# Optimization experiments

Measured on AMD Instinct MI355X. Metric: run time of the kernel, lower is better.

The kernel has to match this reference:

```python
import jax, jax.numpy as jnp
import numpy as np

B, S, V, E, H, C = 64, 512, 30000, 300, 256, 32


def setup_inputs() -> dict:
    key = jax.random.key(0)
    ks = jax.random.split(key, 12)
    g = 0.02
    return dict(
        tokens=jax.random.randint(ks[0], (B, S), 1, V),
        lengths=jax.random.randint(ks[1], (B,), S // 2, S + 1),
        targets=jax.random.randint(ks[2], (B, S), 0, C),
        emb=jax.random.normal(ks[3], (V, E), jnp.float32) * g,
        Wf=jax.random.normal(ks[4], (E, 4 * H), jnp.float32) * g,
        Uf=jax.random.normal(ks[5], (H, 4 * H), jnp.float32) * g,
        bf=jnp.zeros((4 * H,), jnp.float32),
        Wb=jax.random.normal(ks[6], (E, 4 * H), jnp.float32) * g,
        Ub=jax.random.normal(ks[7], (H, 4 * H), jnp.float32) * g,
        bb=jnp.zeros((4 * H,), jnp.float32),
        Wd=jax.random.normal(ks[8], (2 * H, C), jnp.float32) * g,
        bd=jnp.zeros((C,), jnp.float32),
        trans=jax.random.uniform(ks[9], (C, C), jnp.float32),
    )


def _lstm(x, W, U, b):
    # x: [B,S,E] -> hidden sequence [B,S,H]; Keras gate order i,f,g(cand),o
    xproj = jnp.einsum('bse,eh->bsh', x, W) + b  # precompute input projection

    def step(carry, xp):  # xp: [B,4H]
        h, c = carry
        z = xp + h @ U
        i, f, g, o = jnp.split(z, 4, axis=-1)
        c = jax.nn.sigmoid(f) * c + jax.nn.sigmoid(i) * jnp.tanh(g)
        h = jax.nn.sigmoid(o) * jnp.tanh(c)
        return (h, c), h

    h0 = jnp.zeros((x.shape[0], U.shape[0]), x.dtype)
    _, hs = jax.lax.scan(step, (h0, h0), jnp.swapaxes(xproj, 0, 1))
    return jnp.swapaxes(hs, 0, 1)


def _crf_log_likelihood(logits, targets, lengths, trans):
    # tfa.text.crf_log_likelihood: sequence score minus log partition (forward algorithm)
    mask = jnp.arange(S)[None, :] < lengths[:, None]  # [B,S]
    maskf = mask.astype(logits.dtype)
    unary = jnp.take_along_axis(logits, targets[..., None], axis=2)[..., 0]  # [B,S]
    unary = jnp.sum(unary * maskf, axis=1)
    binary = trans[targets[:, :-1], targets[:, 1:]] * maskf[:, 1:]  # valid where t+1 < length
    binary = jnp.sum(binary, axis=1)

    alpha0 = logits[:, 0]  # [B,C] (lengths >= 1)

    def step(alpha, inp):
        logit_t, m_t = inp  # [B,C], [B]
        new = jax.nn.logsumexp(alpha[:, :, None] + trans[None], axis=1) + logit_t
        return jnp.where(m_t[:, None], new, alpha), None

    alpha, _ = jax.lax.scan(
        step, alpha0,
        (jnp.swapaxes(logits[:, 1:], 0, 1), jnp.swapaxes(mask[:, 1:], 0, 1)))
    log_norm = jax.nn.logsumexp(alpha, axis=-1)
    return unary + binary - log_norm


def reference(tokens, lengths, targets, emb, Wf, Uf, bf, Wb, Ub, bb, Wd, bd, trans):
    x = emb[tokens]                         # [B,S,E]; dropout is identity at inference
    hf = _lstm(x, Wf, Uf, bf)               # forward direction
    hb = _lstm(x[:, ::-1], Wb, Ub, bb)[:, ::-1]  # backward direction
    h = jnp.concatenate([hf, hb], axis=-1)  # [B,S,2H]
    logits = h @ Wd + bd                    # [B,S,C]
    ll = _crf_log_likelihood(logits, targets, lengths, trans)
    return logits, ll, trans
```

## Files before the change

### kernel.cpp

```cpp
#include <hip/hip_runtime.h>

#define Bdim 64
#define Sdim 512
#define Vdim 30000
#define Edim 300
#define Hdim 256
#define Cdim 32
#define G4   1024
#define NROW 32768
#define KQ   32
#define USTAGE 9
#define RKQ    12
#define EPAIR  (Edim / 2)
#define KCH    5

typedef _Float16 half2v __attribute__((ext_vector_type(2)));
typedef _Float16 f16x8  __attribute__((ext_vector_type(8)));
typedef float    f32x4  __attribute__((ext_vector_type(4)));
typedef unsigned int u32x4 __attribute__((ext_vector_type(4)));

__device__ __forceinline__ unsigned short f2h_bits(float f) {
    union { _Float16 h; unsigned short u; } v; v.h = (_Float16)f; return v.u;
}
__device__ __forceinline__ float h2f(unsigned short u) {
    union { _Float16 h; unsigned short u; } v; v.u = u; return (float)v.h;
}
__device__ __forceinline__ unsigned int pack2h(float lo, float hi) {
    return (unsigned int)f2h_bits(lo) | ((unsigned int)f2h_bits(hi) << 16);
}
__device__ __forceinline__ float sigf(float x) { return 1.0f / (1.0f + __expf(-x)); }
__device__ __forceinline__ float tanhfast(float x) { return 2.0f / (1.0f + __expf(-2.0f * x)) - 1.0f; }

__device__ __forceinline__ float dot2(unsigned int u, unsigned int h, float acc) {
#if __has_builtin(__builtin_amdgcn_fdot2)
    union { unsigned int i; half2v h; } a, b; a.i = u; b.i = h;
    return __builtin_amdgcn_fdot2(a.h, b.h, acc, false);
#else
    acc = fmaf(h2f((unsigned short)(u & 0xffffu)), h2f((unsigned short)(h & 0xffffu)), acc);
    return fmaf(h2f((unsigned short)(u >> 16)), h2f((unsigned short)(h >> 16)), acc);
#endif
}
__device__ __forceinline__ void dot8(float& a0, float& a1, u32x4 uv, u32x4 hv) {
    a0 = dot2(uv.x, hv.x, a0);
    a1 = dot2(uv.y, hv.y, a1);
    a0 = dot2(uv.z, hv.z, a0);
    a1 = dot2(uv.w, hv.w, a1);
}

__global__ __launch_bounds__(256) void k_pack_u8(
    const float* __restrict__ Uf, const float* __restrict__ Ub,
    unsigned short* __restrict__ upk8)
{
    int idx = blockIdx.x * 256 + threadIdx.x;
    if (idx >= 2 * KQ * 1024) return;
    int dir = idx >> 15;
    int rem = idx & 32767;
    int kq  = rem >> 10;
    int n   = rem & 1023;
    const float* U = dir ? Ub : Uf;
    unsigned int w[4];
    #pragma unroll
    for (int p = 0; p < 4; ++p)
        w[p] = pack2h(U[(8 * kq + 2 * p) * G4 + n], U[(8 * kq + 2 * p + 1) * G4 + n]);
    uint4 o = make_uint4(w[0], w[1], w[2], w[3]);
    *(uint4*)&upk8[(size_t)idx * 8] = o;
}

__global__ __launch_bounds__(256) void k_pack_emb(
    const float* __restrict__ emb, unsigned int* __restrict__ embp)
{
    int p = blockIdx.x * 256 + threadIdx.x;
    if (p >= Vdim * EPAIR) return;
    float2 v = *(const float2*)&emb[(size_t)2 * p];
    embp[p] = pack2h(v.x, v.y);
}

__global__ __launch_bounds__(256) void k_pack_w(
    const float* __restrict__ Wf, const float* __restrict__ Wb,
    unsigned int* __restrict__ Wp)
{
    int idx = blockIdx.x * 256 + threadIdx.x;
    if (idx >= 2 * EPAIR * 1024) return;
    int dir = idx / (EPAIR * 1024);
    int rem = idx - dir * (EPAIR * 1024);
    int kp  = rem >> 10;
    int n   = rem & 1023;
    const float* W = dir ? Wb : Wf;
    Wp[idx] = pack2h(W[(2 * kp) * G4 + n], W[(2 * kp + 1) * G4 + n]);
}

__global__ __launch_bounds__(256) void k_pack_wd(
    const float* __restrict__ Wd, unsigned int* __restrict__ WdP)
{
    int i = blockIdx.x * 256 + threadIdx.x;
    if (i >= 256 * 32) return;
    int kp = i >> 5, c = i & 31;
    WdP[i] = pack2h(Wd[(2 * kp) * 32 + c], Wd[(2 * kp + 1) * 32 + c]);
}

__global__ __launch_bounds__(256, 4) void k_xproj(
    const int* __restrict__ tokens, const unsigned int* __restrict__ embp,
    const unsigned int* __restrict__ Wp,
    const float* __restrict__ bf_, const float* __restrict__ bb_,
    unsigned short* __restrict__ xp)
{
    __shared__ unsigned short As[64][72];
    __shared__ unsigned short Bs[128][72];
    __shared__ int tokL[64];

    const int m0  = blockIdx.x * 64;
    const int n0  = blockIdx.y * 128;
    const int dir = blockIdx.z;
    const unsigned int* W = Wp + (size_t)dir * EPAIR * 1024;
    const float* bias = dir ? bb_ : bf_;
    const int tid = threadIdx.x;

    if (tid < 64) tokL[tid] = tokens[m0 + tid];
    __syncthreads();

    const int w    = tid >> 6;
    const int wm   = w >> 1;
    const int wn   = w & 1;
    const int lane = tid & 63;
    const int lr   = lane & 15;
    const int lh   = lane >> 4;

    f32x4 acc[2][4] = {};

    float bv[4];
    #pragma unroll
    for (int nt = 0; nt < 4; ++nt)
        bv[nt] = bias[n0 + wn * 64 + nt * 16 + lr];

    for (int kc = 0; kc < KCH; ++kc) {
        const int k0p = kc * 32;
        if (kc) __syncthreads();

        {
            const int r  = tid >> 2;
            const int jb = (tid & 3) * 8;
            const int tok = tokL[r];
            unsigned int* dst = (unsigned int*)&As[r][0];
            #pragma unroll
            for (int q = 0; q < 8; ++q) {
                int gp = k0p + jb + q;
                dst[jb + q] = (gp < EPAIR) ? embp[(size_t)tok * EPAIR + gp] : 0u;
            }
        }
        {
            #pragma unroll
            for (int q = 0; q < 16; ++q) {
                int ii = q * 256 + tid;
                int jp = ii >> 7;
                int c  = ii & 127;
                int gp = k0p + jp;
                unsigned int v = (gp < EPAIR) ? W[(size_t)gp * 1024 + n0 + c] : 0u;
                ((unsigned int*)&Bs[c][0])[jp] = v;
            }
        }
        __syncthreads();

        f16x8 a[2][2];
        #pragma unroll
        for (int mt = 0; mt < 2; ++mt)
            #pragma unroll
            for (int ks = 0; ks < 2; ++ks)
                a[mt][ks] = *(const f16x8*)&As[wm * 32 + mt * 16 + lr][ks * 32 + lh * 8];
        #pragma unroll
        for (int nt = 0; nt < 4; ++nt) {
            f16x8 b0 = *(const f16x8*)&Bs[wn * 64 + nt * 16 + lr][lh * 8];
            f16x8 b1 = *(const f16x8*)&Bs[wn * 64 + nt * 16 + lr][32 + lh * 8];
            #pragma unroll
            for (int mt = 0; mt < 2; ++mt) {
                acc[mt][nt] = __builtin_amdgcn_mfma_f32_16x16x32_f16(a[mt][0], b0, acc[mt][nt], 0, 0, 0);
                acc[mt][nt] = __builtin_amdgcn_mfma_f32_16x16x32_f16(a[mt][1], b1, acc[mt][nt], 0, 0, 0);
            }
        }
    }

    size_t base = (size_t)dir * NROW * G4;
    #pragma unroll
    for (int mt = 0; mt < 2; ++mt) {
        #pragma unroll
        for (int nt = 0; nt < 4; ++nt) {
            int col = n0 + wn * 64 + nt * 16 + lr;
            #pragma unroll
            for (int rr = 0; rr < 4; ++rr) {
                int row = m0 + wm * 32 + mt * 16 + lh * 4 + rr;
                xp[base + (size_t)row * G4 + col] = f2h_bits(acc[mt][nt][rr] + bv[nt]);
            }
        }
    }
}

__global__ __launch_bounds__(1024) void k_lstm(
    const unsigned short* __restrict__ upk8,
    const unsigned short* __restrict__ xp,
    unsigned short* __restrict__ hout)
{
    const int bx  = blockIdx.x;
    const int dir = bx >> 6;
    const int b   = bx & 63;
    const int n   = threadIdx.x;
    const int gi  = n >> 8;
    const unsigned short* __restrict__ Uq = upk8 + (size_t)dir * (KQ * 1024 * 8);
    const unsigned short* __restrict__ xpd =
        xp + (size_t)dir * NROW * G4 + (size_t)b * Sdim * G4;

    __shared__ float          abuf[1024];
    __shared__ __align__(16) unsigned short hl[256];
    extern __shared__ __align__(16) unsigned short ust[];

    {
        const u32x4* src = (const u32x4*)Uq;
        u32x4*       dst = (u32x4*)ust;
        for (int i = n; i < USTAGE * 1024; i += 1024) dst[i] = src[i];
    }
    u32x4 ur[RKQ];
    #pragma unroll
    for (int r = 0; r < RKQ; ++r)
        ur[r] = *(const u32x4*)&Uq[((size_t)(USTAGE + r) * 1024 + n) * 8];

    if (n < 256) hl[n] = 0;
    float c = 0.0f;
    __syncthreads();

    for (int step = 0; step < Sdim; ++step) {
        const int t = dir ? (Sdim - 1 - step) : step;
        float zx = h2f(xpd[(size_t)t * G4 + n]);
        float a0 = 0.0f, a1 = 0.0f;
        #pragma unroll
        for (int kq = USTAGE + RKQ; kq < KQ; ++kq) {
            u32x4 uv = *(const u32x4*)&Uq[((size_t)kq * 1024 + n) * 8];
            u32x4 hv = *(const u32x4*)&hl[kq * 8];
            dot8(a0, a1, uv, hv);
        }
        #pragma unroll
        for (int r = 0; r < RKQ; ++r) {
            u32x4 hv = *(const u32x4*)&hl[(USTAGE + r) * 8];
            dot8(a0, a1, ur[r], hv);
        }
        #pragma unroll
        for (int kq = 0; kq < USTAGE; ++kq) {
            u32x4 uv = *(const u32x4*)&ust[(kq * 1024 + n) * 8];
            u32x4 hv = *(const u32x4*)&hl[kq * 8];
            dot8(a0, a1, uv, hv);
        }
        float z = zx + a0 + a1;
        float a = (gi == 2) ? tanhfast(z) : sigf(z);
        abuf[n] = a;
        __syncthreads();
        if (n < 256) {
            float iv = abuf[n];
            float fv = abuf[n + 256];
            float gv = abuf[n + 512];
            float ov = abuf[n + 768];
            c = fv * c + iv * gv;
            float hn = ov * tanhfast(c);
            unsigned short hb = f2h_bits(hn);
            hl[n] = hb;
            hout[((size_t)(b * Sdim + t)) * 512 + dir * 256 + n] = hb;
        }
        __syncthreads();
    }
}

__global__ __launch_bounds__(256) void k_dense(
    const unsigned short* __restrict__ hall, const unsigned int* __restrict__ WdP,
    const float* __restrict__ bd, float* __restrict__ outL)
{
    __shared__ unsigned int wlT[32 * 260];
    __shared__ unsigned int hu[8 * 256];
    const int r0  = blockIdx.x * 8;
    const int tid = threadIdx.x;

    for (int i = tid; i < 256 * 32; i += 256) {
        int kp = i >> 5, c = i & 31;
        wlT[c * 260 + kp] = WdP[i];
    }
    const unsigned int* hsrc = (const unsigned int*)(hall + (size_t)r0 * 512);
    for (int i = tid; i < 8 * 256; i += 256) hu[i] = hsrc[i];
    __syncthreads();

    const int tx = tid & 31, ty = tid >> 5;
    float a0 = 0.0f, a1 = 0.0f;
    #pragma unroll 8
    for (int kp = 0; kp < 256; kp += 4) {
        u32x4 hv = *(const u32x4*)&hu[ty * 256 + kp];
        u32x4 wv = *(const u32x4*)&wlT[tx * 260 + kp];
        a0 = dot2(wv.x, hv.x, a0);
        a1 = dot2(wv.y, hv.y, a1);
        a0 = dot2(wv.z, hv.z, a0);
        a1 = dot2(wv.w, hv.w, a1);
    }
    outL[(size_t)(r0 + ty) * 32 + tx] = a0 + a1 + bd[tx];
}

__global__ __launch_bounds__(64) void k_crf(
    const float* __restrict__ logits, const int* __restrict__ targets,
    const int* __restrict__ lengths, const float* __restrict__ trans,
    float* __restrict__ out_ll, float* __restrict__ out_trans)
{
    const int b    = blockIdx.x;
    const int lane = threadIdx.x;
    __shared__ __align__(16) float alpha[32];

    if (b == 0)
        for (int i = lane; i < 1024; i += 64) out_trans[i] = trans[i];

    const int len = lengths[b];
    const float* lg = logits + (size_t)b * Sdim * Cdim;
    const int*   tg = targets + b * Sdim;

    float ub = 0.0f;
    for (int t = lane; t < Sdim; t += 64) {
        if (t < len) {
            ub += lg[t * 32 + tg[t]];
            if (t >= 1) ub += trans[tg[t - 1] * 32 + tg[t]];
        }
    }
    #pragma unroll
    for (int m = 32; m >= 1; m >>= 1) ub += __shfl_xor(ub, m);

    const int j = lane & 31, half = lane >> 5;
    float trow16[16];
    #pragma unroll
    for (int q = 0; q < 16; ++q) trow16[q] = trans[(half * 16 + q) * 32 + j];

    if (lane < 32) alpha[lane] = lg[lane];
    __syncthreads();

    float lcur = (len > 1) ? lg[32 + j] : 0.0f;
    for (int t = 1; t < len; ++t) {
        float lnxt = (t + 1 < len) ? lg[(t + 1) * 32 + j] : 0.0f;
        float v[16];
        #pragma unroll
        for (int q = 0; q < 16; ++q) v[q] = alpha[half * 16 + q] + trow16[q];
        float m0 = v[0], m1 = v[1], m2 = v[2], m3 = v[3];
        #pragma unroll
        for (int q = 4; q < 16; q += 4) {
            m0 = fmaxf(m0, v[q]);
            m1 = fmaxf(m1, v[q + 1]);
            m2 = fmaxf(m2, v[q + 2]);
            m3 = fmaxf(m3, v[q + 3]);
        }
        float ml = fmaxf(fmaxf(m0, m1), fmaxf(m2, m3));
        float m  = fmaxf(ml, __shfl_xor(ml, 32));
        float s0 = 0.0f, s1 = 0.0f, s2 = 0.0f, s3 = 0.0f;
        #pragma unroll
        for (int q = 0; q < 16; q += 4) {
            s0 += __expf(v[q] - m);
            s1 += __expf(v[q + 1] - m);
            s2 += __expf(v[q + 2] - m);
            s3 += __expf(v[q + 3] - m);
        }
        float sl = (s0 + s1) + (s2 + s3);
        float s  = sl + __shfl_xor(sl, 32);
        float nv = m + __logf(s) + lcur;
        __syncthreads();
        if (lane < 32) alpha[lane] = nv;
        __syncthreads();
        lcur = lnxt;
    }
    if (lane == 0) {
        float m = -3.0e38f;
        for (int q = 0; q < 32; ++q) m = fmaxf(m, alpha[q]);
        float s = 0.0f;
        for (int q = 0; q < 32; ++q) s += __expf(alpha[q] - m);
        out_ll[b] = ub - (m + __logf(s));
    }
}

extern "C" void kernel_launch(void* const* d_in, const int* in_sizes, int n_in,
                              void* d_out, int out_size, void* d_ws, size_t ws_size,
                              hipStream_t stream) {
    (void)in_sizes; (void)n_in; (void)out_size; (void)ws_size;
    const int*   tokens  = (const int*)d_in[0];
    const int*   lengths = (const int*)d_in[1];
    const int*   targets = (const int*)d_in[2];
    const float* emb     = (const float*)d_in[3];
    const float* Wf      = (const float*)d_in[4];
    const float* Uf      = (const float*)d_in[5];
    const float* bf_     = (const float*)d_in[6];
    const float* Wb      = (const float*)d_in[7];
    const float* Ub      = (const float*)d_in[8];
    const float* bb_     = (const float*)d_in[9];
    const float* Wd      = (const float*)d_in[10];
    const float* bd      = (const float*)d_in[11];
    const float* trans   = (const float*)d_in[12];

    float* out_logits = (float*)d_out;
    float* out_ll     = out_logits + 1048576;
    float* out_trans  = out_ll + 64;

    char* ws = (char*)d_ws;
    unsigned short* upk8 = (unsigned short*)ws;
    unsigned short* xp   = (unsigned short*)(ws + (1u << 20));
    char*           hreg = ws + (1u << 20) + (size_t)2 * NROW * G4 * 2;
    unsigned short* hall = (unsigned short*)hreg;
    unsigned int*   embp = (unsigned int*)hreg;
    unsigned int*   Wp   = (unsigned int*)(hreg + (size_t)Vdim * EPAIR * 4);
    unsigned int*   WdP  = (unsigned int*)ws;

    const size_t lstm_dyn_lds = (size_t)USTAGE * 1024 * 8 * 2;

    k_pack_u8 <<<dim3(256), dim3(256), 0, stream>>>(Uf, Ub, upk8);
    k_pack_emb<<<dim3((Vdim * EPAIR + 255) / 256), dim3(256), 0, stream>>>(emb, embp);
    k_pack_w  <<<dim3((2 * EPAIR * 1024 + 255) / 256), dim3(256), 0, stream>>>(Wf, Wb, Wp);
    k_xproj   <<<dim3(NROW / 64, 8, 2), dim3(256), 0, stream>>>(tokens, embp, Wp, bf_, bb_, xp);
    k_lstm    <<<dim3(128), dim3(1024), lstm_dyn_lds, stream>>>(upk8, xp, hall);
    k_pack_wd <<<dim3(32), dim3(256), 0, stream>>>(Wd, WdP);
    k_dense   <<<dim3(NROW / 8), dim3(256), 0, stream>>>(hall, WdP, bd, out_logits);
    k_crf     <<<dim3(64), dim3(64), 0, stream>>>(out_logits, targets, lengths, trans, out_ll, out_trans);
}
```

Measured before the change: 1.179 ms.

## Use MFMA for dense logits and shuffle-based alpha in CRF

The dense projection now has each block handle 64 rows, and each wave computes a 16x32 tile with f16 MFMA instructions that read rows directly from global memory. This replaces the per-thread dot2 loop and its LDS staging of h, and loads the Wd tile once per 64 rows instead of once per 8. Separately, the CRF forward recursion keeps alpha in a register and broadcasts it with wave shuffles, which removes two __syncthreads and the LDS round trip on every timestep. Both kernels are small next to the LSTM recurrence, so the effect on total time is likely minor.

Measured after the change: 1.206 ms. +2.2%, slower.

```diff
diff --git a/kernel.cpp b/kernel.cpp
--- a/kernel.cpp
+++ b/kernel.cpp
@@ -265,35 +265,47 @@
     }
 }
 
-__global__ __launch_bounds__(256) void k_dense(
+__global__ __launch_bounds__(256, 4) void k_dense(
     const unsigned short* __restrict__ hall, const unsigned int* __restrict__ WdP,
     const float* __restrict__ bd, float* __restrict__ outL)
 {
     __shared__ unsigned int wlT[32 * 260];
-    __shared__ unsigned int hu[8 * 256];
-    const int r0  = blockIdx.x * 8;
+    const int r0  = blockIdx.x * 64;
     const int tid = threadIdx.x;
 
     for (int i = tid; i < 256 * 32; i += 256) {
         int kp = i >> 5, c = i & 31;
         wlT[c * 260 + kp] = WdP[i];
     }
-    const unsigned int* hsrc = (const unsigned int*)(hall + (size_t)r0 * 512);
-    for (int i = tid; i < 8 * 256; i += 256) hu[i] = hsrc[i];
     __syncthreads();
 
-    const int tx = tid & 31, ty = tid >> 5;
-    float a0 = 0.0f, a1 = 0.0f;
-    #pragma unroll 8
-    for (int kp = 0; kp < 256; kp += 4) {
-        u32x4 hv = *(const u32x4*)&hu[ty * 256 + kp];
-        u32x4 wv = *(const u32x4*)&wlT[tx * 260 + kp];
-        a0 = dot2(wv.x, hv.x, a0);
-        a1 = dot2(wv.y, hv.y, a1);
-        a0 = dot2(wv.z, hv.z, a0);
-        a1 = dot2(wv.w, hv.w, a1);
-    }
-    outL[(size_t)(r0 + ty) * 32 + tx] = a0 + a1 + bd[tx];
+    const int w    = tid >> 6;
+    const int lane = tid & 63;
+    const int lr   = lane & 15;
+    const int lh   = lane >> 4;
+
+    const unsigned short* arow = hall + (size_t)(r0 + w * 16 + lr) * 512;
+    f32x4 acc[2] = {};
+
+    #pragma unroll
+    for (int kc = 0; kc < 16; ++kc) {
+        f16x8 av = *(const f16x8*)&arow[kc * 32 + lh * 8];
+        f16x8 b0 = *(const f16x8*)((const unsigned int*)wlT + lr * 260 + kc * 16 + lh * 4);
+        f16x8 b1 = *(const f16x8*)((const unsigned int*)wlT + (16 + lr) * 260 + kc * 16 + lh * 4);
+        acc[0] = __builtin_amdgcn_mfma_f32_16x16x32_f16(av, b0, acc[0], 0, 0, 0);
+        acc[1] = __builtin_amdgcn_mfma_f32_16x16x32_f16(av, b1, acc[1], 0, 0, 0);
+    }
+
+    #pragma unroll
+    for (int nt = 0; nt < 2; ++nt) {
+        int col = nt * 16 + lr;
+        float bdv = bd[col];
+        #pragma unroll
+        for (int rr = 0; rr < 4; ++rr) {
+            int row = r0 + w * 16 + lh * 4 + rr;
+            outL[(size_t)row * 32 + col] = acc[nt][rr] + bdv;
+        }
+    }
 }
 
 __global__ __launch_bounds__(64) void k_crf(
@@ -303,7 +315,6 @@
 {
     const int b    = blockIdx.x;
     const int lane = threadIdx.x;
-    __shared__ __align__(16) float alpha[32];
 
     if (b == 0)
         for (int i = lane; i < 1024; i += 64) out_trans[i] = trans[i];
@@ -327,15 +338,15 @@
     #pragma unroll
     for (int q = 0; q < 16; ++q) trow16[q] = trans[(half * 16 + q) * 32 + j];
 
-    if (lane < 32) alpha[lane] = lg[lane];
-    __syncthreads();
+    float alpha = lg[j];
 
     float lcur = (len > 1) ? lg[32 + j] : 0.0f;
     for (int t = 1; t < len; ++t) {
         float lnxt = (t + 1 < len) ? lg[(t + 1) * 32 + j] : 0.0f;
         float v[16];
         #pragma unroll
-        for (int q = 0; q < 16; ++q) v[q] = alpha[half * 16 + q] + trow16[q];
+        for (int q = 0; q < 16; ++q)
+            v[q] = __shfl(alpha, half * 16 + q) + trow16[q];
         float m0 = v[0], m1 = v[1], m2 = v[2], m3 = v[3];
         #pragma unroll
         for (int q = 4; q < 16; q += 4) {
@@ -356,19 +367,14 @@
         }
         float sl = (s0 + s1) + (s2 + s3);
         float s  = sl + __shfl_xor(sl, 32);
-        float nv = m + __logf(s) + lcur;
-        __syncthreads();
-        if (lane < 32) alpha[lane] = nv;
-        __syncthreads();
+        alpha = m + __logf(s) + lcur;
         lcur = lnxt;
     }
-    if (lane == 0) {
-        float m = -3.0e38f;
-        for (int q = 0; q < 32; ++q) m = fmaxf(m, alpha[q]);
-        float s = 0.0f;
-        for (int q = 0; q < 32; ++q) s += __expf(alpha[q] - m);
-        out_ll[b] = ub - (m + __logf(s));
-    }
+    float mf = -3.0e38f;
+    for (int q = 0; q < 32; ++q) mf = fmaxf(mf, __shfl(alpha, q));
+    float sf = 0.0f;
+    for (int q = 0; q < 32; ++q) sf += __expf(__shfl(alpha, q) - mf);
+    if (lane == 0) out_ll[b] = ub - (mf + __logf(sf));
 }
 
 extern "C" void kernel_launch(void* const* d_in, const int* in_sizes, int n_in,
@@ -410,6 +416,6 @@
     k_xproj   <<<dim3(NROW / 64, 8, 2), dim3(256), 0, stream>>>(tokens, embp, Wp, bf_, bb_, xp);
     k_lstm    <<<dim3(128), dim3(1024), lstm_dyn_lds, stream>>>(upk8, xp, hall);
     k_pack_wd <<<dim3(32), dim3(256), 0, stream>>>(Wd, WdP);
-    k_dense   <<<dim3(NROW / 8), dim3(256), 0, stream>>>(hall, WdP, bd, out_logits);
+    k_dense   <<<dim3(NROW / 64), dim3(256), 0, stream>>>(hall, WdP, bd, out_logits);
     k_crf     <<<dim3(64), dim3(64), 0, stream>>>(out_logits, targets, lengths, trans, out_ll, out_trans);
 }
```
